# Kernel optimization log

Measured on AMD Instinct MI355X. Metric: run time of the kernel, lower is better.

Reference implementation:

```python
import jax, jax.numpy as jnp
import numpy as np

H = 16          # num_heads
EPS = 1e-6      # RMSNorm eps


def _rms_norm(t, w):
    # t: [..., head_dim], w: [head_dim]
    var = jnp.mean(jnp.square(t), axis=-1, keepdims=True)
    return t * jax.lax.rsqrt(var + EPS) * w


def setup_inputs() -> dict:
    key = jax.random.key(0)
    ks = jax.random.split(key, 8)
    B, N, M, C = 2, 2048, 256, 1024
    s = 0.02
    return {
        "x": jax.random.normal(ks[0], (B, N, C), jnp.float32),
        "y": jax.random.normal(ks[1], (B, M, C), jnp.float32),
        "qkv_w": jax.random.normal(ks[2], (3 * C, C), jnp.float32) * s,
        "qkv_b": jax.random.normal(ks[3], (3 * C,), jnp.float32) * s,
        "kv_w": jax.random.normal(ks[4], (2 * C, C), jnp.float32) * s,
        "kv_b": jax.random.normal(ks[5], (2 * C,), jnp.float32) * s,
        "qn_w": jnp.ones((C // H,), jnp.float32),
        "kn_w": jnp.ones((C // H,), jnp.float32),
        "proj_w": jax.random.normal(ks[6], (C, C), jnp.float32) * s,
        "proj_b": jax.random.normal(ks[7], (C,), jnp.float32) * s,
    }


def reference(x, y, qkv_w, qkv_b, kv_w, kv_b, qn_w, kn_w, proj_w, proj_b):
    B, N, C = x.shape
    M = y.shape[1]
    hd = C // H
    scale = hd ** -0.5

    # fused QKV projection for image tokens -> [B, H, N, hd] each
    qkv = (jnp.einsum('bnc,oc->bno', x, qkv_w) + qkv_b).reshape(B, N, 3, H, hd)
    qkv = jnp.transpose(qkv, (2, 0, 3, 1, 4))
    q, kx, vx = qkv[0], qkv[1], qkv[2]

    # qk-norm (RMSNorm over head_dim)
    q = _rms_norm(q, qn_w)
    kx = _rms_norm(kx, kn_w)

    # KV projection for text tokens -> [B, H, M, hd] each
    kvy = (jnp.einsum('bmc,oc->bmo', y, kv_w) + kv_b).reshape(B, M, 2, H, hd)
    kvy = jnp.transpose(kvy, (2, 0, 3, 1, 4))
    ky, vy = kvy[0], kvy[1]
    ky = _rms_norm(ky, kn_w)

    # concat image+text KV along the sequence axis
    k = jnp.concatenate([kx, ky], axis=2)  # [B, H, N+M, hd]
    v = jnp.concatenate([vx, vy], axis=2)

    # scaled dot-product attention
    logits = jnp.einsum('bhnd,bhsd->bhns', q, k) * scale  # [B, H, N, N+M]
    attn = jax.nn.softmax(logits, axis=-1)
    out = jnp.einsum('bhns,bhsd->bhnd', attn, v)          # [B, H, N, hd]

    out = jnp.transpose(out, (0, 2, 1, 3)).reshape(B, N, C)
    return jnp.einsum('bnc,oc->bno', out, proj_w) + proj_b
```

## Files before the change

### kernel.cpp

```cpp
#include <hip/hip_runtime.h>

#define BATCH 2
#define NTOK 2048
#define MTOK 256
#define CDIM 1024
#define NHEAD 16
#define HD 64
#define SEQ (NTOK + MTOK)
#define TOK_X (BATCH * NTOK)
#define TOK_Y (BATCH * MTOK)
#define BHN (BATCH * NHEAD)
#define NKT (SEQ / 64)

typedef __attribute__((ext_vector_type(8))) short bf16x8;
typedef __attribute__((ext_vector_type(4))) short bf16x4;
typedef __attribute__((ext_vector_type(4))) float f32x4;
typedef __attribute__((ext_vector_type(2))) unsigned int u32x2;
typedef __attribute__((ext_vector_type(4))) unsigned int u32x4;
#if __has_builtin(__builtin_amdgcn_cvt_pk_bf16_f32)
typedef __attribute__((ext_vector_type(2))) __bf16 bf16x2_t;
#endif

__device__ __forceinline__ float b2f(ushort u) {
    unsigned v = ((unsigned)u) << 16;
    return __builtin_bit_cast(float, v);
}
__device__ __forceinline__ ushort f2b(float f) {
    unsigned u = __builtin_bit_cast(unsigned, f);
    u += 0x7fffu + ((u >> 16) & 1u);
    return (ushort)(u >> 16);
}
__device__ __forceinline__ unsigned pack2bf(float a, float b) {
#if __has_builtin(__builtin_amdgcn_cvt_pk_bf16_f32)
    bf16x2_t h = __builtin_amdgcn_cvt_pk_bf16_f32(a, b);
    return __builtin_bit_cast(unsigned, h);
#else
    return ((unsigned)f2b(b) << 16) | (unsigned)f2b(a);
#endif
}

__device__ __forceinline__ void async_load16(const ushort* g, ushort* l) {
    __builtin_amdgcn_global_load_lds(
        (const __attribute__((address_space(1))) unsigned*)(const void*)g,
        (__attribute__((address_space(3))) unsigned*)(void*)l, 16, 0, 0);
}

__global__ __launch_bounds__(256) void cast_all(
    const float* __restrict__ s0, ushort* __restrict__ t0, int b0,
    const float* __restrict__ s1, ushort* __restrict__ t1, int b1,
    const float* __restrict__ s2, ushort* __restrict__ t2, int b2,
    const float* __restrict__ s3, ushort* __restrict__ t3, int b3,
    const float* __restrict__ s4, ushort* __restrict__ t4) {
    int blk = blockIdx.x;
    const float* s; ushort* t;
    if (blk < b0)      { s = s0; t = t0; }
    else if (blk < b1) { s = s1; t = t1; blk -= b0; }
    else if (blk < b2) { s = s2; t = t2; blk -= b1; }
    else if (blk < b3) { s = s3; t = t3; blk -= b2; }
    else               { s = s4; t = t4; blk -= b3; }
    int i = (blk * 256 + threadIdx.x) * 8;
    float4 a = *(const float4*)(s + i);
    float4 b = *(const float4*)(s + i + 4);
    ushort tmp[8] = {f2b(a.x), f2b(a.y), f2b(a.z), f2b(a.w),
                     f2b(b.x), f2b(b.y), f2b(b.z), f2b(b.w)};
    *(uint4*)(t + i) = *(const uint4*)tmp;
}

template <int MODE>
__global__ __launch_bounds__(256) void gemm_fused(const ushort* __restrict__ A,
                                                  const ushort* __restrict__ Bt,
                                                  const float* __restrict__ bias,
                                                  float* __restrict__ Cf,
                                                  ushort* __restrict__ d_q,
                                                  ushort* __restrict__ d_k,
                                                  ushort* __restrict__ d_v,
                                                  const float* __restrict__ qn_w,
                                                  const float* __restrict__ kn_w,
                                                  int M, int N, int K) {
    __shared__ ushort As[128][64];
    __shared__ ushort Bs[128][64];
    int tid = threadIdx.x;
    int lane = tid & 63;
    int w = tid >> 6;
    int wm = (w >> 1) * 64;
    int wn = (w & 1) * 64;
    int l15 = lane & 15;
    int quad = lane >> 4;
    int sw = l15 & 7;
    int bm = blockIdx.y * 128;
    int bn = blockIdx.x * 128;

    f32x4 acc[4][4];
#pragma unroll
    for (int i = 0; i < 4; i++)
#pragma unroll
        for (int j = 0; j < 4; j++) acc[i][j] = (f32x4)0.0f;

    int lrow = lane >> 3;
    int lcol = ((lane & 7) ^ lrow) * 8;

    for (int k0 = 0; k0 < K; k0 += 64) {
        __syncthreads();
#pragma unroll
        for (int p = 0; p < 4; p++) {
            int rb = w * 32 + p * 8;
            async_load16(&A[(size_t)(bm + rb + lrow) * K + k0 + lcol], &As[rb][0]);
            async_load16(&Bt[(size_t)(bn + rb + lrow) * K + k0 + lcol], &Bs[rb][0]);
        }
        __syncthreads();
#pragma unroll
        for (int kk = 0; kk < 64; kk += 32) {
            bf16x8 af[4], bfr[4];
            int g = (kk >> 3) + quad;
            int csw = (g ^ sw) * 8;
#pragma unroll
            for (int i = 0; i < 4; i++)
                af[i] = *(const bf16x8*)&As[wm + i * 16 + l15][csw];
#pragma unroll
            for (int j = 0; j < 4; j++)
                bfr[j] = *(const bf16x8*)&Bs[wn + j * 16 + l15][csw];
#pragma unroll
            for (int i = 0; i < 4; i++)
#pragma unroll
                for (int j = 0; j < 4; j++)
                    acc[i][j] = __builtin_amdgcn_mfma_f32_16x16x32_bf16(af[i], bfr[j], acc[i][j], 0, 0, 0);
        }
    }

    int colbase = bn + wn;
    float bv[4];
#pragma unroll
    for (int j = 0; j < 4; j++) bv[j] = bias[colbase + j * 16 + l15];
#pragma unroll
    for (int i = 0; i < 4; i++)
#pragma unroll
        for (int j = 0; j < 4; j++)
#pragma unroll
            for (int r = 0; r < 4; r++) acc[i][j][r] += bv[j];

    if (MODE == 0) {
#pragma unroll
        for (int i = 0; i < 4; i++) {
            int row0 = bm + wm + i * 16 + quad * 4;
#pragma unroll
            for (int j = 0; j < 4; j++) {
                int col = colbase + j * 16 + l15;
#pragma unroll
                for (int r = 0; r < 4; r++)
                    Cf[(size_t)(row0 + r) * N + col] = acc[i][j][r];
            }
        }
        return;
    }

    int region = colbase >> 10;
    int h = (colbase >> 6) & (NHEAD - 1);
    bool do_norm = (MODE == 1) ? (region <= 1) : (region == 0);
    if (do_norm) {
        const float* wv = (MODE == 1 && region == 0) ? qn_w : kn_w;
        float wj[4];
#pragma unroll
        for (int j = 0; j < 4; j++) wj[j] = wv[j * 16 + l15];
        float qs = (MODE == 1 && region == 0) ? (0.125f * 1.44269504088896f) : 1.0f;
#pragma unroll
        for (int i = 0; i < 4; i++)
#pragma unroll
            for (int r = 0; r < 4; r++) {
                float s = acc[i][0][r] * acc[i][0][r] + acc[i][1][r] * acc[i][1][r]
                        + acc[i][2][r] * acc[i][2][r] + acc[i][3][r] * acc[i][3][r];
                s += __shfl_xor(s, 1);
                s += __shfl_xor(s, 2);
                s += __shfl_xor(s, 4);
                s += __shfl_xor(s, 8);
                float rs = rsqrtf(s * (1.0f / 64.0f) + 1e-6f) * qs;
#pragma unroll
                for (int j = 0; j < 4; j++) acc[i][j][r] *= rs * wj[j];
            }
    }
#pragma unroll
    for (int i = 0; i < 4; i++) {
#pragma unroll
        for (int r = 0; r < 4; r++) {
            int t = bm + wm + i * 16 + quad * 4 + r;
            size_t base;
            ushort* dst;
            if (MODE == 1) {
                int b = t >> 11, n = t & (NTOK - 1);
                size_t bh = (size_t)(b * NHEAD + h);
                if (region == 0)      { dst = d_q; base = (bh * NTOK + n) * 64; }
                else if (region == 1) { dst = d_k; base = (bh * SEQ + n) * 64; }
                else                  { dst = d_v; base = (bh * SEQ + n) * 64; }
            } else {
                int b = t >> 8, m = t & (MTOK - 1);
                size_t bh = (size_t)(b * NHEAD + h);
                if (region == 0) { dst = d_k; base = (bh * SEQ + NTOK + m) * 64; }
                else             { dst = d_v; base = (bh * SEQ + NTOK + m) * 64; }
            }
#pragma unroll
            for (int j = 0; j < 4; j++)
                dst[base + j * 16 + l15] = f2b(acc[i][j][r]);
        }
    }
}

__global__ __launch_bounds__(256) void transpose_v(const ushort* __restrict__ vc,
                                                   ushort* __restrict__ vt) {
    __shared__ ushort t[64][72];
    int bh = blockIdx.y;
    int s0 = blockIdx.x * 64;
    int tid = threadIdx.x;
    int r = tid >> 3, c = (tid & 7) * 8;
    const ushort* src = vc + ((size_t)bh * SEQ + s0) * 64;
    *(uint4*)&t[r][c] = *(const uint4*)&src[(size_t)r * 64 + c];
    *(uint4*)&t[r + 32][c] = *(const uint4*)&src[(size_t)(r + 32) * 64 + c];
    __syncthreads();
    ushort* dst = vt + (size_t)bh * 64 * SEQ + s0;
#pragma unroll
    for (int p = 0; p < 2; p++) {
        int d = (tid >> 3) + p * 32;
        int s8 = (tid & 7) * 8;
        ushort tmp[8];
#pragma unroll
        for (int i = 0; i < 8; i++) {
            int cc = s8 + i;
            int srcs = (cc & 32) + ((cc & 31) >> 1) + ((cc & 1) << 4);
            tmp[i] = t[srcs][d];
        }
        *(uint4*)&dst[(size_t)d * SEQ + s8] = *(const uint4*)tmp;
    }
}

__global__ __launch_bounds__(256) void attn_fwd(const ushort* __restrict__ qh,
                                                const ushort* __restrict__ kc,
                                                const ushort* __restrict__ vt,
                                                ushort* __restrict__ out) {
    __shared__ ushort Ks[2][64][72];
    __shared__ ushort Vs[2][64][68];
    int tid = threadIdx.x;
    int lane = tid & 63;
    int w = tid >> 6;
    int l15 = lane & 15;
    int quad = lane >> 4;
    int bh = blockIdx.y;
    int q0 = blockIdx.x * 128 + w * 32;

    const ushort* qpA = qh + ((size_t)bh * NTOK + q0 + l15) * 64 + quad * 8;
    const ushort* qpB = qpA + 16 * 64;
    bf16x8 qA0 = *(const bf16x8*)qpA;
    bf16x8 qA1 = *(const bf16x8*)(qpA + 32);
    bf16x8 qB0 = *(const bf16x8*)qpB;
    bf16x8 qB1 = *(const bf16x8*)(qpB + 32);

    float lA = 0.0f, lB = 0.0f;
    f32x4 OA[4], OB[4];
#pragma unroll
    for (int jd = 0; jd < 4; jd++) { OA[jd] = (f32x4)0.0f; OB[jd] = (f32x4)0.0f; }

    const ushort* kbase = kc + (size_t)bh * SEQ * 64;
    const ushort* vbase = vt + (size_t)bh * 64 * SEQ;
    int sr = tid >> 3, sc = (tid & 7) * 8;
    const ushort* kp0 = kbase + (size_t)sr * 64 + sc;
    const ushort* kp1 = kbase + (size_t)(sr + 32) * 64 + sc;
    const ushort* vp0 = vbase + (size_t)sr * SEQ + sc;
    const ushort* vp1 = vbase + (size_t)(sr + 32) * SEQ + sc;

    uint4 rka = *(const uint4*)kp0;
    uint4 rkb = *(const uint4*)kp1;
    uint4 rva = *(const uint4*)vp0;
    uint4 rvb = *(const uint4*)vp1;

    for (int t = 0; t < NKT; t++) {
        int p = t & 1;
        *(uint4*)&Ks[p][sr][sc] = rka;
        *(uint4*)&Ks[p][sr + 32][sc] = rkb;
        *(uint4*)&Vs[p][sr][sc] = rva;
        *(uint4*)&Vs[p][sr + 32][sc] = rvb;
        __syncthreads();
        if (t + 1 < NKT) {
            int s0 = (t + 1) * 64;
            rka = *(const uint4*)(kp0 + (size_t)s0 * 64);
            rkb = *(const uint4*)(kp1 + (size_t)s0 * 64);
            rva = *(const uint4*)(vp0 + s0);
            rvb = *(const uint4*)(vp1 + s0);
        }

        f32x4 SA[4], SB[4];
#pragma unroll
        for (int j = 0; j < 4; j++) { SA[j] = (f32x4)0.0f; SB[j] = (f32x4)0.0f; }
#pragma unroll
        for (int j = 0; j < 4; j++) {
            bf16x8 kf = *(const bf16x8*)&Ks[p][j * 16 + l15][quad * 8];
            SA[j] = __builtin_amdgcn_mfma_f32_16x16x32_bf16(kf, qA0, SA[j], 0, 0, 0);
            SB[j] = __builtin_amdgcn_mfma_f32_16x16x32_bf16(kf, qB0, SB[j], 0, 0, 0);
        }
#pragma unroll
        for (int j = 0; j < 4; j++) {
            bf16x8 kf = *(const bf16x8*)&Ks[p][j * 16 + l15][32 + quad * 8];
            SA[j] = __builtin_amdgcn_mfma_f32_16x16x32_bf16(kf, qA1, SA[j], 0, 0, 0);
            SB[j] = __builtin_amdgcn_mfma_f32_16x16x32_bf16(kf, qB1, SB[j], 0, 0, 0);
        }

#pragma unroll
        for (int pb2 = 0; pb2 < 2; pb2++) {
            int j0 = 2 * pb2, j1 = j0 + 1;
            u32x4 wa, wb;
#pragma unroll
            for (int r = 0; r < 4; r++) {
                float a0 = __builtin_amdgcn_exp2f(SA[j0][r]);
                float a1 = __builtin_amdgcn_exp2f(SA[j1][r]);
                lA += a0 + a1;
                wa[r] = pack2bf(a0, a1);
                float b0 = __builtin_amdgcn_exp2f(SB[j0][r]);
                float b1 = __builtin_amdgcn_exp2f(SB[j1][r]);
                lB += b0 + b1;
                wb[r] = pack2bf(b0, b1);
            }
            bf16x8 pA = __builtin_bit_cast(bf16x8, wa);
            bf16x8 pB = __builtin_bit_cast(bf16x8, wb);
#pragma unroll
            for (int jd = 0; jd < 4; jd++) {
                bf16x8 vf = *(const bf16x8*)&Vs[p][jd * 16 + l15][pb2 * 32 + quad * 8];
                OA[jd] = __builtin_amdgcn_mfma_f32_16x16x32_bf16(vf, pA, OA[jd], 0, 0, 0);
                OB[jd] = __builtin_amdgcn_mfma_f32_16x16x32_bf16(vf, pB, OB[jd], 0, 0, 0);
            }
        }
    }
    lA += __shfl_xor(lA, 16);
    lA += __shfl_xor(lA, 32);
    lB += __shfl_xor(lB, 16);
    lB += __shfl_xor(lB, 32);
    float invA = 1.0f / lA;
    float invB = 1.0f / lB;
    int b = bh >> 4, h = bh & 15;
    int tokA = (b << 11) + q0 + l15;
    ushort* obaseA = out + ((size_t)tokA * NHEAD + h) * 64;
    ushort* obaseB = obaseA + (size_t)16 * NHEAD * 64;
#pragma unroll
    for (int jd = 0; jd < 4; jd++) {
        u32x2 pk;
        pk.x = pack2bf(OA[jd][0] * invA, OA[jd][1] * invA);
        pk.y = pack2bf(OA[jd][2] * invA, OA[jd][3] * invA);
        *(u32x2*)&obaseA[jd * 16 + quad * 4] = pk;
        pk.x = pack2bf(OB[jd][0] * invB, OB[jd][1] * invB);
        pk.y = pack2bf(OB[jd][2] * invB, OB[jd][3] * invB);
        *(u32x2*)&obaseB[jd * 16 + quad * 4] = pk;
    }
}

extern "C" void kernel_launch(void* const* d_in, const int* in_sizes, int n_in,
                              void* d_out, int out_size, void* d_ws, size_t ws_size,
                              hipStream_t stream) {
    const float* x      = (const float*)d_in[0];
    const float* y      = (const float*)d_in[1];
    const float* qkv_w  = (const float*)d_in[2];
    const float* qkv_b  = (const float*)d_in[3];
    const float* kv_w   = (const float*)d_in[4];
    const float* kv_b   = (const float*)d_in[5];
    const float* qn_w   = (const float*)d_in[6];
    const float* kn_w   = (const float*)d_in[7];
    const float* proj_w = (const float*)d_in[8];
    const float* proj_b = (const float*)d_in[9];
    float* outp = (float*)d_out;

    char* ws = (char*)d_ws;
    ushort* x_bf    = (ushort*)ws; ws += (size_t)TOK_X * CDIM * 2;
    ushort* y_bf    = (ushort*)ws; ws += (size_t)TOK_Y * CDIM * 2;
    ushort* qkvw_bf = (ushort*)ws; ws += (size_t)3 * CDIM * CDIM * 2;
    ushort* kvw_bf  = (ushort*)ws; ws += (size_t)2 * CDIM * CDIM * 2;
    ushort* projw_bf= (ushort*)ws; ws += (size_t)CDIM * CDIM * 2;
    ushort* qh      = (ushort*)ws; ws += (size_t)BHN * NTOK * 64 * 2;
    ushort* kc      = (ushort*)ws; ws += (size_t)BHN * SEQ * 64 * 2;
    ushort* vc      = (ushort*)ws; ws += (size_t)BHN * SEQ * 64 * 2;
    ushort* vt      = (ushort*)ws; ws += (size_t)BHN * SEQ * 64 * 2;
    ushort* ao      = (ushort*)ws; ws += (size_t)TOK_X * CDIM * 2;

    int c0 = TOK_X * CDIM / 2048;
    int c1 = c0 + TOK_Y * CDIM / 2048;
    int c2 = c1 + 3 * CDIM * CDIM / 2048;
    int c3 = c2 + 2 * CDIM * CDIM / 2048;
    int c4 = c3 + CDIM * CDIM / 2048;
    cast_all<<<c4, 256, 0, stream>>>(x, x_bf, c0, y, y_bf, c1, qkv_w, qkvw_bf, c2,
                                     kv_w, kvw_bf, c3, proj_w, projw_bf);

    gemm_fused<1><<<dim3(3 * CDIM / 128, TOK_X / 128), 256, 0, stream>>>(
        x_bf, qkvw_bf, qkv_b, nullptr, qh, kc, vc, qn_w, kn_w, TOK_X, 3 * CDIM, CDIM);
    gemm_fused<2><<<dim3(2 * CDIM / 128, TOK_Y / 128), 256, 0, stream>>>(
        y_bf, kvw_bf, kv_b, nullptr, nullptr, kc, vc, qn_w, kn_w, TOK_Y, 2 * CDIM, CDIM);

    transpose_v<<<dim3(SEQ / 64, BHN), 256, 0, stream>>>(vc, vt);

    attn_fwd<<<dim3(NTOK / 128, BHN), 256, 0, stream>>>(qh, kc, vt, ao);

    gemm_fused<0><<<dim3(CDIM / 128, TOK_X / 128), 256, 0, stream>>>(
        ao, projw_bf, proj_b, outp, nullptr, nullptr, nullptr, nullptr, nullptr,
        TOK_X, CDIM, CDIM);
}
```

Baseline: 252.9 us.

## Split attention over two key halves and combine partial outputs in a new kernel

Attention blocks now each process half of the key sequence, doubling the grid, and write unnormalized partial outputs plus row sums to workspace. A new combine kernel sums the two halves and normalizes by the total row sum. This targets underutilization of the CUs with the original grid size, at the cost of an extra launch, extra memory traffic for partial results, and bf16 rounding of unnormalized partials.

```diff
diff --git a/kernel.cpp b/kernel.cpp
--- a/kernel.cpp
+++ b/kernel.cpp
@@ -11,6 +11,8 @@
 #define TOK_Y (BATCH * MTOK)
 #define BHN (BATCH * NHEAD)
 #define NKT (SEQ / 64)
+#define HALFKEYS (SEQ / 2)
+#define NKTH (NKT / 2)
 
 typedef __attribute__((ext_vector_type(8))) short bf16x8;
 typedef __attribute__((ext_vector_type(4))) short bf16x4;
@@ -233,7 +235,8 @@
 __global__ __launch_bounds__(256) void attn_fwd(const ushort* __restrict__ qh,
                                                 const ushort* __restrict__ kc,
                                                 const ushort* __restrict__ vt,
-                                                ushort* __restrict__ out) {
+                                                ushort* __restrict__ po,
+                                                float* __restrict__ pl) {
     __shared__ ushort Ks[2][64][72];
     __shared__ ushort Vs[2][64][68];
     int tid = threadIdx.x;
@@ -241,7 +244,9 @@
     int w = tid >> 6;
     int l15 = lane & 15;
     int quad = lane >> 4;
-    int bh = blockIdx.y;
+    int bhh = blockIdx.y;
+    int half = bhh & 1;
+    int bh = bhh >> 1;
     int q0 = blockIdx.x * 128 + w * 32;
 
     const ushort* qpA = qh + ((size_t)bh * NTOK + q0 + l15) * 64 + quad * 8;
@@ -256,8 +261,8 @@
 #pragma unroll
     for (int jd = 0; jd < 4; jd++) { OA[jd] = (f32x4)0.0f; OB[jd] = (f32x4)0.0f; }
 
-    const ushort* kbase = kc + (size_t)bh * SEQ * 64;
-    const ushort* vbase = vt + (size_t)bh * 64 * SEQ;
+    const ushort* kbase = kc + ((size_t)bh * SEQ + half * HALFKEYS) * 64;
+    const ushort* vbase = vt + (size_t)bh * 64 * SEQ + half * HALFKEYS;
     int sr = tid >> 3, sc = (tid & 7) * 8;
     const ushort* kp0 = kbase + (size_t)sr * 64 + sc;
     const ushort* kp1 = kbase + (size_t)(sr + 32) * 64 + sc;
@@ -269,14 +274,14 @@
     uint4 rva = *(const uint4*)vp0;
     uint4 rvb = *(const uint4*)vp1;
 
-    for (int t = 0; t < NKT; t++) {
+    for (int t = 0; t < NKTH; t++) {
         int p = t & 1;
         *(uint4*)&Ks[p][sr][sc] = rka;
         *(uint4*)&Ks[p][sr + 32][sc] = rkb;
         *(uint4*)&Vs[p][sr][sc] = rva;
         *(uint4*)&Vs[p][sr + 32][sc] = rvb;
         __syncthreads();
-        if (t + 1 < NKT) {
+        if (t + 1 < NKTH) {
             int s0 = (t + 1) * 64;
             rka = *(const uint4*)(kp0 + (size_t)s0 * 64);
             rkb = *(const uint4*)(kp1 + (size_t)s0 * 64);
@@ -329,22 +334,50 @@
     lA += __shfl_xor(lA, 32);
     lB += __shfl_xor(lB, 16);
     lB += __shfl_xor(lB, 32);
-    float invA = 1.0f / lA;
-    float invB = 1.0f / lB;
     int b = bh >> 4, h = bh & 15;
     int tokA = (b << 11) + q0 + l15;
-    ushort* obaseA = out + ((size_t)tokA * NHEAD + h) * 64;
+    ushort* obaseA = po + (size_t)half * TOK_X * CDIM + ((size_t)tokA * NHEAD + h) * 64;
     ushort* obaseB = obaseA + (size_t)16 * NHEAD * 64;
 #pragma unroll
     for (int jd = 0; jd < 4; jd++) {
         u32x2 pk;
-        pk.x = pack2bf(OA[jd][0] * invA, OA[jd][1] * invA);
-        pk.y = pack2bf(OA[jd][2] * invA, OA[jd][3] * invA);
+        pk.x = pack2bf(OA[jd][0], OA[jd][1]);
+        pk.y = pack2bf(OA[jd][2], OA[jd][3]);
         *(u32x2*)&obaseA[jd * 16 + quad * 4] = pk;
-        pk.x = pack2bf(OB[jd][0] * invB, OB[jd][1] * invB);
-        pk.y = pack2bf(OB[jd][2] * invB, OB[jd][3] * invB);
+        pk.x = pack2bf(OB[jd][0], OB[jd][1]);
+        pk.y = pack2bf(OB[jd][2], OB[jd][3]);
         *(u32x2*)&obaseB[jd * 16 + quad * 4] = pk;
     }
+    if (lane < 16) {
+        float* plh = pl + (size_t)(half * BHN + bh) * NTOK;
+        plh[q0 + l15] = lA;
+        plh[q0 + 16 + l15] = lB;
+    }
+}
+
+__global__ __launch_bounds__(256) void combine_halves(const ushort* __restrict__ po,
+                                                      const float* __restrict__ pl,
+                                                      ushort* __restrict__ ao) {
+    int idx = (blockIdx.x * 256 + threadIdx.x) * 8;
+    int tok = idx >> 10;
+    int c = idx & (CDIM - 1);
+    int h = c >> 6;
+    int b = tok >> 11, n = tok & (NTOK - 1);
+    int bh = b * NHEAD + h;
+    float l = pl[(size_t)bh * NTOK + n] + pl[(size_t)(BHN + bh) * NTOK + n];
+    float inv = 1.0f / l;
+    uint4 a0 = *(const uint4*)&po[idx];
+    uint4 a1 = *(const uint4*)&po[(size_t)TOK_X * CDIM + idx];
+    const ushort* u0 = (const ushort*)&a0;
+    const ushort* u1 = (const ushort*)&a1;
+    unsigned outw[4];
+#pragma unroll
+    for (int i = 0; i < 4; i++) {
+        float e0 = (b2f(u0[2 * i]) + b2f(u1[2 * i])) * inv;
+        float e1 = (b2f(u0[2 * i + 1]) + b2f(u1[2 * i + 1])) * inv;
+        outw[i] = pack2bf(e0, e1);
+    }
+    *(uint4*)&ao[idx] = *(const uint4*)outw;
 }
 
 extern "C" void kernel_launch(void* const* d_in, const int* in_sizes, int n_in,
@@ -373,6 +406,8 @@
     ushort* vc      = (ushort*)ws; ws += (size_t)BHN * SEQ * 64 * 2;
     ushort* vt      = (ushort*)ws; ws += (size_t)BHN * SEQ * 64 * 2;
     ushort* ao      = (ushort*)ws; ws += (size_t)TOK_X * CDIM * 2;
+    ushort* po      = (ushort*)ws; ws += (size_t)2 * TOK_X * CDIM * 2;
+    float*  pl      = (float*)ws;  ws += (size_t)2 * BHN * NTOK * 4;
 
     int c0 = TOK_X * CDIM / 2048;
     int c1 = c0 + TOK_Y * CDIM / 2048;
@@ -389,7 +424,8 @@
 
     transpose_v<<<dim3(SEQ / 64, BHN), 256, 0, stream>>>(vc, vt);
 
-    attn_fwd<<<dim3(NTOK / 128, BHN), 256, 0, stream>>>(qh, kc, vt, ao);
+    attn_fwd<<<dim3(NTOK / 128, BHN * 2), 256, 0, stream>>>(qh, kc, vt, po, pl);
+    combine_halves<<<TOK_X * CDIM / 2048, 256, 0, stream>>>(po, pl, ao);
 
     gemm_fused<0><<<dim3(CDIM / 128, TOK_X / 128), 256, 0, stream>>>(
         ao, projw_bf, proj_b, outp, nullptr, nullptr, nullptr, nullptr, nullptr,
```

After: 261.6 us. 3.4% more time.
